# Kernel tuning notes

Hardware: AMD Instinct MI355X
Metric: run time of the kernel (lower is better)

Reference implementation:

```python
import jax, jax.numpy as jnp
import numpy as np

L, D, V = 8, 1024, 32000
DT_MIN, DT_MAX = 0.01, 0.1
EPS = 1e-5


def _layer_norm(x, w, b):
    mu = jnp.mean(x, -1, keepdims=True)
    var = jnp.var(x, -1, keepdims=True)
    return (x - mu) * jax.lax.rsqrt(var + EPS) * w + b


def _encode(ids):
    # deterministic phase encoding of tokens onto the unit phase sphere
    theta = 2.0 * jnp.pi * ids.astype(jnp.float32) / V  # [B,S]
    k = jnp.arange(1, D // 2 + 1, dtype=jnp.float32)
    ang = theta[..., None] * k  # [B,S,D/2]
    return jnp.concatenate([jnp.cos(ang), jnp.sin(ang)], -1) / jnp.sqrt(jnp.float32(D))


def _flux(s, mask):
    # attention-like causal score from state self-interaction
    score = jnp.einsum('bqd,bkd->bqk', s, s) / jnp.sqrt(jnp.float32(D))
    score = jnp.where(mask, score, 0.0)
    return jnp.einsum('bqk,bkd->bqd', score, s), score


def _evolve_with_tunneling(s, dt, mask):
    # Heun-Euler (predictor-corrector) integration step
    k1, score = _flux(s, mask)
    mid = s + dt * k1
    k2, _ = _flux(mid, mask)
    ev = s + 0.5 * dt * (k1 + k2)
    # quantum tunneling: boost low-energy states proportionally to dt/dt_max
    energy = jnp.linalg.norm(ev, axis=-1)  # [B,S]
    thr = jnp.mean(energy, axis=-1, keepdims=True)
    tunnel = energy < thr
    strength = dt / DT_MAX  # [B,1,1]
    ev = jnp.where(tunnel[..., None], ev * (1.0 + strength), ev)
    ratio = jnp.mean(tunnel.astype(jnp.float32))
    return ev, score, ratio


def setup_inputs() -> dict:
    key = jax.random.key(0)
    ks = jax.random.split(key, 4)
    B, S = 2, 2048
    input_ids = jax.random.randint(ks[0], (B, S), 0, V)
    labels = jax.random.randint(ks[1], (B, S), 0, V)
    proj_w = jax.random.normal(ks[2], (L, D, D), jnp.float32) * 0.02
    proj_b = jnp.zeros((L, D), jnp.float32)
    ln_w = jnp.ones((L, D), jnp.float32)
    ln_b = jnp.zeros((L, D), jnp.float32)
    fln_w = jnp.ones((D,), jnp.float32)
    fln_b = jnp.zeros((D,), jnp.float32)
    out_w = jax.random.normal(ks[3], (D, V), jnp.float32) * 0.02
    return dict(input_ids=input_ids, labels=labels, proj_w=proj_w, proj_b=proj_b,
                ln_w=ln_w, ln_b=ln_b, fln_w=fln_w, fln_b=fln_b, out_w=out_w)


def reference(input_ids, labels, proj_w, proj_b, ln_w, ln_b, fln_w, fln_b, out_w):
    B, S = input_ids.shape
    mask = jnp.tril(jnp.ones((S, S), dtype=bool))
    # deterministic timestep (midpoint of [dt_min, dt_max]); dropout in eval mode
    dt = jnp.full((B, 1, 1), 0.5 * (DT_MIN + DT_MAX), jnp.float32)
    states = _encode(input_ids)
    for i in range(L):
        ev, _score, _ratio = _evolve_with_tunneling(states, dt, mask)
        states = _layer_norm(ev @ proj_w[i] + proj_b[i], ln_w[i], ln_b[i])
    states = _layer_norm(states, fln_w, fln_b)
    # normalized quantum projection to vocab
    energy = jnp.linalg.norm(states, axis=-1, keepdims=True)
    logits = (states / (energy + 1e-12)) @ out_w  # [B,S,V]
    # shifted cross-entropy
    sl = logits[:, :-1, :].reshape(-1, V)
    tl = labels[:, 1:].reshape(-1)
    logp = jax.nn.log_softmax(sl, axis=-1)
    loss = -jnp.mean(jnp.take_along_axis(logp, tl[:, None], axis=1))
    return logits, loss
```

## Files before the change

kernel.cpp:

```cpp
#include <hip/hip_runtime.h>

#define LL 8
#define DD 1024
#define VV 32000
#define SS 2048
#define BB 2
#define NROWS 4096
#define DT_STEP 0.055f
#define HALF_DT 0.0275f
#define TUNNEL_SCALE 1.55f

typedef __attribute__((ext_vector_type(8))) short bf16x8;
typedef __attribute__((ext_vector_type(4))) float f32x4;

static __device__ __forceinline__ float bf2f(unsigned short u){
  union { unsigned int i; float f; } v; v.i = ((unsigned int)u) << 16; return v.f;
}
static __device__ __forceinline__ unsigned short f2bf(float f){
  union { float f; unsigned int i; } v; v.f = f;
  unsigned int r = v.i + 0x7fffu + ((v.i >> 16) & 1u);
  return (unsigned short)(r >> 16);
}

static __device__ __forceinline__ void gl16(const unsigned short* g, unsigned short* l){
  __builtin_amdgcn_global_load_lds(
      (const __attribute__((address_space(1))) unsigned int*)g,
      (__attribute__((address_space(3))) unsigned int*)l, 16, 0, 0);
}

__device__ __forceinline__ float block_sum256(float v, volatile float* scratch){
  #pragma unroll
  for (int off = 32; off; off >>= 1) v += __shfl_down(v, off, 64);
  int w = threadIdx.x >> 6, lane = threadIdx.x & 63;
  __syncthreads();
  if (lane == 0) scratch[w] = v;
  __syncthreads();
  return scratch[0] + scratch[1] + scratch[2] + scratch[3];
}

__global__ void encode_kernel(const int* __restrict__ ids, float* __restrict__ s_f32,
                              unsigned short* __restrict__ hi, unsigned short* __restrict__ lo){
  int row = blockIdx.x;
  int t = threadIdx.x;
  float theta = 6.28318530717958647692f * (float)ids[row] / 32000.0f;
  #pragma unroll
  for (int i = 0; i < 2; ++i){
    int kk = t + i * 256;
    float ang = theta * (float)(kk + 1);
    float sv, cv; sincosf(ang, &sv, &cv);
    float c = cv * 0.03125f, s = sv * 0.03125f;
    long b0 = (long)row * DD + kk, b1 = b0 + 512;
    s_f32[b0] = c; s_f32[b1] = s;
    unsigned short ch = f2bf(c); hi[b0] = ch; lo[b0] = f2bf(c - bf2f(ch));
    unsigned short sh = f2bf(s); hi[b1] = sh; lo[b1] = f2bf(s - bf2f(sh));
  }
}

__global__ void transpose_bf16_pair_kernel(const unsigned short* __restrict__ in_hi,
                                           const unsigned short* __restrict__ in_lo,
                                           unsigned short* __restrict__ out_hi,
                                           unsigned short* __restrict__ out_lo,
                                           int R, int C){
  __shared__ __align__(16) unsigned short tile[64][80];
  int zz = blockIdx.z;
  const unsigned short* in = (zz & 1) ? in_lo : in_hi;
  unsigned short* out = (zz & 1) ? out_lo : out_hi;
  long ib = (long)(zz >> 1) * R * C;
  int c0 = blockIdx.x * 64, r0 = blockIdx.y * 64;
  int t = threadIdx.x;
  #pragma unroll
  for (int i = 0; i < 2; ++i){
    int j = t + i * 256; int row = j >> 3, cc = j & 7;
    *(uint4*)&tile[row][cc * 8] = *(const uint4*)(in + ib + (long)(r0 + row) * C + c0 + cc * 8);
  }
  __syncthreads();
  #pragma unroll
  for (int i = 0; i < 2; ++i){
    int j = t + i * 256; int orow = j >> 3, cc = j & 7;
    union { unsigned short u[8]; uint4 v; } tmp;
    #pragma unroll
    for (int e = 0; e < 8; ++e) tmp.u[e] = tile[cc * 8 + e][orow];
    *(uint4*)(out + ib + (long)(c0 + orow) * R + r0 + cc * 8) = tmp.v;
  }
}

template<bool SPLIT>
__global__ void transpose_f32_bf16_kernel(const float* __restrict__ in,
                                          unsigned short* __restrict__ ohi,
                                          unsigned short* __restrict__ olo, int R, int C){
  __shared__ float tile[64][68];
  long ib = (long)blockIdx.z * R * C;
  int c0 = blockIdx.x * 64, r0 = blockIdx.y * 64;
  int t = threadIdx.x;
  #pragma unroll
  for (int i = 0; i < 4; ++i){
    int j = t + i * 256; int row = j >> 4, cc = j & 15;
    *(float4*)&tile[row][cc * 4] = *(const float4*)(in + ib + (long)(r0 + row) * C + c0 + cc * 4);
  }
  __syncthreads();
  #pragma unroll
  for (int i = 0; i < 2; ++i){
    int j = t + i * 256; int orow = j >> 3, cc = j & 7;
    union { unsigned short u[8]; uint4 v; } th, tl;
    #pragma unroll
    for (int e = 0; e < 8; ++e){
      float v = tile[cc * 8 + e][orow];
      unsigned short h = f2bf(v); th.u[e] = h;
      if (SPLIT) tl.u[e] = f2bf(v - bf2f(h));
    }
    long ob = ib + (long)(c0 + orow) * R + r0 + cc * 8;
    *(uint4*)(ohi + ob) = th.v;
    if (SPLIT) *(uint4*)(olo + ob) = tl.v;
  }
}

template<int OUTMODE, int CAUSAL>
__global__ __launch_bounds__(512, 4)
void gemm_nt_kernel(const unsigned short* __restrict__ Ahi, const unsigned short* __restrict__ Alo,
                    const unsigned short* __restrict__ Bhi, const unsigned short* __restrict__ Blo,
                    float* __restrict__ C, unsigned short* __restrict__ Chi,
                    unsigned short* __restrict__ Clo, const float* __restrict__ bias,
                    const float* __restrict__ Sf, const float* __restrict__ K1f,
                    int K, int lda, int ldb, int ldc, int MT, int NT,
                    long batchA, long batchB, long batchC, float alpha)
{
  const int bz = blockIdx.y;
  const int nwg = MT * NT;
  const int q = nwg >> 3, r = nwg & 7;
  const int xcd = blockIdx.x & 7, off = blockIdx.x >> 3;
  const int wg = (xcd < r ? xcd * (q + 1) : r * (q + 1) + (xcd - r) * q) + off;
  const int band = wg / (NT << 3), rem = wg - band * (NT << 3);
  const int mt = (band << 3) + (rem & 7), nt = rem >> 3;
  if (CAUSAL == 1 && nt > mt) return;
  const int m0 = mt << 7, n0 = nt << 7;
  int Keff = K;
  if (CAUSAL == 2){ int kl = (mt + 1) << 7; Keff = kl < K ? kl : K; }

  __shared__ __align__(16) unsigned short sA[2][128][64];
  __shared__ __align__(16) unsigned short sB[2][128][64];

  const int tid = threadIdx.x;
  const int lane = tid & 63;
  const int w = tid >> 6;
  const int wr = w >> 2, wc = w & 3;
  const int fr = lane & 15, fc = lane >> 4;
  const int fr7 = fr & 7;

  f32x4 acc[4][2];
  #pragma unroll
  for (int i = 0; i < 4; ++i)
    #pragma unroll
    for (int j = 0; j < 2; ++j) acc[i][j] = (f32x4){0.f, 0.f, 0.f, 0.f};

  const int srow = tid >> 3, slot = tid & 7;
  const int cont = slot ^ (srow & 7);
  const long aoff = (long)bz * batchA, boff = (long)bz * batchB;
  const int gcol = (cont & 3) << 3;
  const unsigned short* gA = (cont >= 4 ? Alo : Ahi) + aoff + (long)(m0 + srow) * lda + gcol;
  const unsigned short* gB = (cont >= 4 ? Blo : Bhi) + boff + (long)(n0 + srow) * ldb + gcol;
  const long rstepA = 64L * lda, rstepB = 64L * ldb;
  const int wofs = w << 9;

  #define STAGE(buf, kt) do {                                        \
    gl16(gA + (kt),          &sA[buf][0][0] + wofs);                 \
    gl16(gA + (kt) + rstepA, &sA[buf][0][0] + 4096 + wofs);          \
    gl16(gB + (kt),          &sB[buf][0][0] + wofs);                 \
    gl16(gB + (kt) + rstepB, &sB[buf][0][0] + 4096 + wofs);          \
  } while(0)

  const int oh = (fc ^ fr7) << 4;
  const int ol = ((4 + fc) ^ fr7) << 4;

  #define COMPUTE(buf) do {                                                         \
    const char* bA_ = (const char*)&sA[buf][0][0];                                  \
    const char* bB_ = (const char*)&sB[buf][0][0];                                  \
    bf16x8 ah_[4], al_[4];                                                          \
    _Pragma("unroll")                                                               \
    for (int mi = 0; mi < 4; ++mi){                                                 \
      const char* p_ = bA_ + (wr * 64 + mi * 16 + fr) * 128;                        \
      ah_[mi] = *(const bf16x8*)(p_ + oh);                                          \
      al_[mi] = *(const bf16x8*)(p_ + ol);                                          \
    }                                                                               \
    _Pragma("unroll")                                                               \
    for (int ni = 0; ni < 2; ++ni){                                                 \
      const char* pb_ = bB_ + (wc * 32 + ni * 16 + fr) * 128;                       \
      bf16x8 bh_ = *(const bf16x8*)(pb_ + oh);                                      \
      bf16x8 bl_ = *(const bf16x8*)(pb_ + ol);                                      \
      _Pragma("unroll")                                                             \
      for (int mi = 0; mi < 4; ++mi){                                               \
        acc[mi][ni] = __builtin_amdgcn_mfma_f32_16x16x32_bf16(ah_[mi], bh_, acc[mi][ni], 0, 0, 0);\
        acc[mi][ni] = __builtin_amdgcn_mfma_f32_16x16x32_bf16(ah_[mi], bl_, acc[mi][ni], 0, 0, 0);\
        acc[mi][ni] = __builtin_amdgcn_mfma_f32_16x16x32_bf16(al_[mi], bh_, acc[mi][ni], 0, 0, 0);\
      }                                                                             \
    }                                                                               \
  } while(0)

  const int ntiles = Keff >> 5;

  STAGE(0, 0);
  int cur = 0;
  for (int t = 0; t < ntiles - 1; ++t){
    asm volatile("s_barrier" ::: "memory");
    STAGE(cur ^ 1, (t + 1) << 5);
    asm volatile("s_waitcnt vmcnt(4)" ::: "memory");
    asm volatile("s_barrier" ::: "memory");
    COMPUTE(cur);
    cur ^= 1;
  }
  asm volatile("s_waitcnt vmcnt(0)" ::: "memory");
  asm volatile("s_barrier" ::: "memory");
  COMPUTE(cur);

  #undef STAGE
  #undef COMPUTE

  const long coff = (long)bz * batchC;
  const int rb0 = m0 + wr * 64 + fc * 4;
  const int cb0 = n0 + wc * 32 + fr;
  #pragma unroll
  for (int mi = 0; mi < 4; ++mi){
    #pragma unroll
    for (int ni = 0; ni < 2; ++ni){
      #pragma unroll
      for (int rg = 0; rg < 4; ++rg){
        int row = rb0 + mi * 16 + rg;
        int col = cb0 + ni * 16;
        float v = acc[mi][ni][rg] * alpha;
        long idx = coff + (long)row * ldc + col;
        if (OUTMODE == 0){
          if (bias) v += bias[col];
          C[idx] = v;
        } else if (OUTMODE == 2){
          if (CAUSAL == 1 && col > row) v = 0.0f;
          unsigned short h = f2bf(v);
          Chi[idx] = h;
          Clo[idx] = f2bf(v - bf2f(h));
        } else if (OUTMODE == 3){
          C[idx] = v;
          float m = Sf[idx] + DT_STEP * v;
          unsigned short h = f2bf(m);
          Chi[idx] = h;
          Clo[idx] = f2bf(m - bf2f(h));
        } else {
          C[idx] = Sf[idx] + HALF_DT * (K1f[idx] + v);
        }
      }
    }
  }
}

__global__ __launch_bounds__(512, 2)
void gemm256_kernel(const unsigned short* __restrict__ A,
                    const unsigned short* __restrict__ Bt,
                    float* __restrict__ C,
                    float* __restrict__ psum)
{
  const int MT = 16, NT = 125;
  const int nwg = MT * NT;
  const int q = nwg >> 3, r = nwg & 7;
  const int xcd = blockIdx.x & 7, off = blockIdx.x >> 3;
  const int wg = (xcd < r ? xcd * (q + 1) : r * (q + 1) + (xcd - r) * q) + off;
  const int band = wg / (NT << 3), rem = wg - band * (NT << 3);
  const int mt = (band << 3) + (rem & 7), nt = rem >> 3;
  const int m0 = mt << 8, n0 = nt << 8;

  __shared__ __align__(16) unsigned short sA[2][256][64];
  __shared__ __align__(16) unsigned short sB[2][256][64];

  const int tid = threadIdx.x;
  const int lane = tid & 63;
  const int w = tid >> 6;
  const int wr = w >> 2, wc = w & 3;
  const int fr = lane & 15, fc = lane >> 4;
  const int fr7 = fr & 7;

  f32x4 acc[8][4];
  #pragma unroll
  for (int i = 0; i < 8; ++i)
    #pragma unroll
    for (int j = 0; j < 4; ++j) acc[i][j] = (f32x4){0.f, 0.f, 0.f, 0.f};

  const int srow = tid >> 3, slot = tid & 7;
  const int cont = slot ^ (srow & 7);
  const unsigned short* gA = A  + (long)(m0 + srow) * DD + (cont << 3);
  const unsigned short* gB = Bt + (long)(n0 + srow) * DD + (cont << 3);
  const int wofs = w << 9;

  #define SGA(buf, kt, i) gl16(gA + (long)((i) * 64) * DD + (kt), &sA[buf][0][0] + (i) * 4096 + wofs)
  #define SGB(buf, kt, i) gl16(gB + (long)((i) * 64) * DD + (kt), &sB[buf][0][0] + (i) * 4096 + wofs)

  const int oh = (fc ^ fr7) << 4;
  const int ol = ((4 + fc) ^ fr7) << 4;

  #pragma unroll
  for (int i = 0; i < 4; ++i){ SGA(0, 0, i); SGB(0, 0, i); }

  int cur = 0;
  for (int t = 0; t < 16; ++t){
    const int nk = (t + 1) << 6;
    const bool stg = (t < 15);
    const char* bA = (const char*)&sA[cur][0][0];
    const char* bB = (const char*)&sB[cur][0][0];
    bf16x8 aq[4][2], bq[4][2];

    if (stg){ SGA(cur ^ 1, nk, 0); SGA(cur ^ 1, nk, 1);
              asm volatile("s_waitcnt vmcnt(2)" ::: "memory"); }
    else    { asm volatile("s_waitcnt vmcnt(0)" ::: "memory"); }
    asm volatile("s_barrier" ::: "memory");
    #pragma unroll
    for (int mi = 0; mi < 4; ++mi){
      const char* p = bA + (wr * 128 + mi * 16 + fr) * 128;
      aq[mi][0] = *(const bf16x8*)(p + oh);
      aq[mi][1] = *(const bf16x8*)(p + ol);
    }
    #pragma unroll
    for (int ni = 0; ni < 2; ++ni){
      const char* p = bB + (wc * 64 + ni * 16 + fr) * 128;
      bq[ni][0] = *(const bf16x8*)(p + oh);
      bq[ni][1] = *(const bf16x8*)(p + ol);
    }
    __builtin_amdgcn_s_setprio(1);
    #pragma unroll
    for (int ks = 0; ks < 2; ++ks)
      #pragma unroll
      for (int mi = 0; mi < 4; ++mi)
        #pragma unroll
        for (int ni = 0; ni < 2; ++ni)
          acc[mi][ni] = __builtin_amdgcn_mfma_f32_16x16x32_bf16(aq[mi][ks], bq[ni][ks], acc[mi][ni], 0, 0, 0);
    __builtin_amdgcn_s_setprio(0);

    if (stg){ SGA(cur ^ 1, nk, 2); SGA(cur ^ 1, nk, 3); }
    asm volatile("s_barrier" ::: "memory");
    #pragma unroll
    for (int ni = 2; ni < 4; ++ni){
      const char* p = bB + (wc * 64 + ni * 16 + fr) * 128;
      bq[ni][0] = *(const bf16x8*)(p + oh);
      bq[ni][1] = *(const bf16x8*)(p + ol);
    }
    __builtin_amdgcn_s_setprio(1);
    #pragma unroll
    for (int ks = 0; ks < 2; ++ks)
      #pragma unroll
      for (int mi = 0; mi < 4; ++mi)
        #pragma unroll
        for (int ni = 2; ni < 4; ++ni)
          acc[mi][ni] = __builtin_amdgcn_mfma_f32_16x16x32_bf16(aq[mi][ks], bq[ni][ks], acc[mi][ni], 0, 0, 0);
    __builtin_amdgcn_s_setprio(0);

    if (stg){ SGB(cur ^ 1, nk, 0); SGB(cur ^ 1, nk, 1); }
    asm volatile("s_barrier" ::: "memory");
    #pragma unroll
    for (int mi = 0; mi < 4; ++mi){
      const char* p = bA + (wr * 128 + (mi + 4) * 16 + fr) * 128;
      aq[mi][0] = *(const bf16x8*)(p + oh);
      aq[mi][1] = *(const bf16x8*)(p + ol);
    }
    __builtin_amdgcn_s_setprio(1);
    #pragma unroll
    for (int ks = 0; ks < 2; ++ks)
      #pragma unroll
      for (int mi = 0; mi < 4; ++mi)
        #pragma unroll
        for (int ni = 2; ni < 4; ++ni)
          acc[mi + 4][ni] = __builtin_amdgcn_mfma_f32_16x16x32_bf16(aq[mi][ks], bq[ni][ks], acc[mi + 4][ni], 0, 0, 0);
    __builtin_amdgcn_s_setprio(0);

    if (stg){ SGB(cur ^ 1, nk, 2); SGB(cur ^ 1, nk, 3); }
    asm volatile("s_barrier" ::: "memory");
    __builtin_amdgcn_s_setprio(1);
    #pragma unroll
    for (int ks = 0; ks < 2; ++ks)
      #pragma unroll
      for (int mi = 0; mi < 4; ++mi)
        #pragma unroll
        for (int ni = 0; ni < 2; ++ni)
          acc[mi + 4][ni] = __builtin_amdgcn_mfma_f32_16x16x32_bf16(aq[mi][ks], bq[ni][ks], acc[mi + 4][ni], 0, 0, 0);
    __builtin_amdgcn_s_setprio(0);

    cur ^= 1;
  }
  #undef SGA
  #undef SGB

  const int rb0 = m0 + wr * 128 + fc * 4;
  const int cb0 = n0 + wc * 64 + fr;
  #pragma unroll
  for (int mi = 0; mi < 8; ++mi){
    #pragma unroll
    for (int ni = 0; ni < 4; ++ni){
      #pragma unroll
      for (int rg = 0; rg < 4; ++rg){
        C[(long)(rb0 + mi * 16 + rg) * VV + cb0 + ni * 16] = acc[mi][ni][rg];
      }
    }
  }

  #pragma unroll
  for (int mi = 0; mi < 8; ++mi){
    #pragma unroll
    for (int rg = 0; rg < 4; ++rg){
      float s4 = __expf(acc[mi][0][rg]) + __expf(acc[mi][1][rg])
               + __expf(acc[mi][2][rg]) + __expf(acc[mi][3][rg]);
      #pragma unroll
      for (int o = 1; o < 16; o <<= 1) s4 += __shfl_xor(s4, o, 64);
      if (fr == 0){
        long pidx = ((long)(rb0 + mi * 16 + rg) << 9) + nt * 4 + wc;
        psum[pidx] = s4;
      }
    }
  }
}

__global__ void energy_kernel(const float* __restrict__ ev, float* __restrict__ energy){
  int row = blockIdx.x, t = threadIdx.x;
  long base = (long)row * DD + t * 4;
  float4 v = *(const float4*)(ev + base);
  __shared__ float scratch[4];
  float n2 = block_sum256(v.x*v.x + v.y*v.y + v.z*v.z + v.w*v.w, scratch);
  if (t == 0) energy[row] = sqrtf(n2);
}

__global__ void mean_energy_kernel(const float* __restrict__ energy, float* __restrict__ thr){
  int b = blockIdx.x, t = threadIdx.x;
  float s = 0.f;
  for (int j = t; j < SS; j += 256) s += energy[b * SS + j];
  __shared__ float scratch[4];
  float tot = block_sum256(s, scratch);
  if (t == 0) thr[b] = tot * (1.0f / SS);
}

__global__ void tunnel_kernel(const float* __restrict__ ev, const float* __restrict__ energy,
                              const float* __restrict__ thr,
                              unsigned short* __restrict__ hi, unsigned short* __restrict__ lo){
  int row = blockIdx.x, t = threadIdx.x;
  float scale = (energy[row] < thr[row >> 11]) ? TUNNEL_SCALE : 1.0f;
  long base = (long)row * DD + t * 4;
  float4 v = *(const float4*)(ev + base);
  v.x *= scale; v.y *= scale; v.z *= scale; v.w *= scale;
  ushort4 hv, lv;
  hv.x = f2bf(v.x); lv.x = f2bf(v.x - bf2f(hv.x));
  hv.y = f2bf(v.y); lv.y = f2bf(v.y - bf2f(hv.y));
  hv.z = f2bf(v.z); lv.z = f2bf(v.z - bf2f(hv.z));
  hv.w = f2bf(v.w); lv.w = f2bf(v.w - bf2f(hv.w));
  *(ushort4*)(hi + base) = hv; *(ushort4*)(lo + base) = lv;
}

__global__ void ln_kernel(const float* __restrict__ h, const float* __restrict__ w,
                          const float* __restrict__ b, float* __restrict__ s_f32,
                          unsigned short* __restrict__ hi, unsigned short* __restrict__ lo){
  int row = blockIdx.x, t = threadIdx.x;
  long base = (long)row * DD + t * 4;
  float4 xv = *(const float4*)(h + base);
  __shared__ float scratch[4];
  float sum = block_sum256(xv.x + xv.y + xv.z + xv.w, scratch);
  float ssq = block_sum256(xv.x*xv.x + xv.y*xv.y + xv.z*xv.z + xv.w*xv.w, scratch);
  float mu = sum * (1.0f / DD);
  float var = ssq * (1.0f / DD) - mu * mu;
  float rstd = rsqrtf(var + 1e-5f);
  float4 wv = *(const float4*)(w + t * 4), bv = *(const float4*)(b + t * 4);
  float y0 = (xv.x - mu) * rstd * wv.x + bv.x;
  float y1 = (xv.y - mu) * rstd * wv.y + bv.y;
  float y2 = (xv.z - mu) * rstd * wv.z + bv.z;
  float y3 = (xv.w - mu) * rstd * wv.w + bv.w;
  float4 o; o.x = y0; o.y = y1; o.z = y2; o.w = y3;
  *(float4*)(s_f32 + base) = o;
  ushort4 hv, lv;
  hv.x = f2bf(y0); lv.x = f2bf(y0 - bf2f(hv.x));
  hv.y = f2bf(y1); lv.y = f2bf(y1 - bf2f(hv.y));
  hv.z = f2bf(y2); lv.z = f2bf(y2 - bf2f(hv.z));
  hv.w = f2bf(y3); lv.w = f2bf(y3 - bf2f(hv.w));
  *(ushort4*)(hi + base) = hv; *(ushort4*)(lo + base) = lv;
}

__global__ void fln_kernel(const float* __restrict__ s, const float* __restrict__ w,
                           const float* __restrict__ b, unsigned short* __restrict__ uhi){
  int row = blockIdx.x, t = threadIdx.x;
  long base = (long)row * DD + t * 4;
  float4 xv = *(const float4*)(s + base);
  __shared__ float scratch[4];
  float sum = block_sum256(xv.x + xv.y + xv.z + xv.w, scratch);
  float ssq = block_sum256(xv.x*xv.x + xv.y*xv.y + xv.z*xv.z + xv.w*xv.w, scratch);
  float mu = sum * (1.0f / DD);
  float var = ssq * (1.0f / DD) - mu * mu;
  float rstd = rsqrtf(var + 1e-5f);
  float4 wv = *(const float4*)(w + t * 4), bv = *(const float4*)(b + t * 4);
  float y0 = (xv.x - mu) * rstd * wv.x + bv.x;
  float y1 = (xv.y - mu) * rstd * wv.y + bv.y;
  float y2 = (xv.z - mu) * rstd * wv.z + bv.z;
  float y3 = (xv.w - mu) * rstd * wv.w + bv.w;
  float n2 = block_sum256(y0*y0 + y1*y1 + y2*y2 + y3*y3, scratch);
  float inv = 1.0f / (sqrtf(n2) + 1e-12f);
  ushort4 o;
  o.x = f2bf(y0 * inv); o.y = f2bf(y1 * inv);
  o.z = f2bf(y2 * inv); o.w = f2bf(y3 * inv);
  *(ushort4*)(uhi + base) = o;
}

__global__ void lse_reduce_kernel(const float* __restrict__ psum,
                                  const float* __restrict__ logits, const int* __restrict__ labels,
                                  float* __restrict__ lrow){
  int idx = blockIdx.x;
  int b = idx / (SS - 1), qq = idx - b * (SS - 1);
  int row = b * SS + qq;
  int t = threadIdx.x;
  float l = 0.f;
  for (int p = t; p < 500; p += 64) l += psum[((long)row << 9) + p];
  #pragma unroll
  for (int o = 1; o < 64; o <<= 1) l += __shfl_xor(l, o, 64);
  if (t == 0){
    float lse = __logf(l);
    float tl = logits[(long)row * VV + labels[row + 1]];
    lrow[idx] = lse - tl;
  }
}

__global__ void loss_reduce_kernel(const float* __restrict__ lrow, float* __restrict__ dst){
  __shared__ float scratch[4];
  float s = 0.f;
  for (int j = threadIdx.x; j < BB * (SS - 1); j += 256) s += lrow[j];
  float tot = block_sum256(s, scratch);
  if (threadIdx.x == 0) dst[0] = tot / (float)(BB * (SS - 1));
}

extern "C" void kernel_launch(void* const* d_in, const int* in_sizes, int n_in,
                              void* d_out, int out_size, void* d_ws, size_t ws_size,
                              hipStream_t stream) {
  const int*   ids    = (const int*)d_in[0];
  const int*   labels = (const int*)d_in[1];
  const float* proj_w = (const float*)d_in[2];
  const float* proj_b = (const float*)d_in[3];
  const float* ln_w   = (const float*)d_in[4];
  const float* ln_b   = (const float*)d_in[5];
  const float* fln_w  = (const float*)d_in[6];
  const float* fln_b  = (const float*)d_in[7];
  const float* out_w  = (const float*)d_in[8];
  float* out = (float*)d_out;

  char* ws = (char*)d_ws;
  float*          s_f32 = (float*)(ws + 0);
  unsigned short* op_hi = (unsigned short*)(ws + 16777216);
  unsigned short* op_lo = (unsigned short*)(ws + 25165824);
  unsigned short* T_hi  = (unsigned short*)(ws + 33554432);
  unsigned short* T_lo  = (unsigned short*)(ws + 41943040);
  float*          k1    = (float*)(ws + 50331648);
  float*          k2    = (float*)(ws + 67108864);
  unsigned short* sc_hi = (unsigned short*)(ws + 83886080);
  unsigned short* sc_lo = (unsigned short*)(ws + 92274688);
  unsigned short* WhiT  = (unsigned short*)(ws + 100663296);
  unsigned short* WloT  = (unsigned short*)(ws + 117440512);
  float*          energy= (float*)(ws + 134217728);
  float*          thr   = (float*)(ws + 134234112);
  float*          lrow  = (float*)(ws + 134234368);
  unsigned short* owT   = T_hi;
  float*          psum  = (float*)(ws + 0);

  transpose_f32_bf16_kernel<true><<<dim3(16, 16, 8), 256, 0, stream>>>(proj_w, WhiT, WloT, DD, DD);
  encode_kernel<<<NROWS, 256, 0, stream>>>(ids, s_f32, op_hi, op_lo);
  transpose_bf16_pair_kernel<<<dim3(16, 32, 4), 256, 0, stream>>>(op_hi, op_lo, T_hi, T_lo, SS, DD);

  for (int l = 0; l < LL; ++l){
    gemm_nt_kernel<2, 1><<<dim3(256, 2), 512, 0, stream>>>(
        op_hi, op_lo, op_hi, op_lo, nullptr, sc_hi, sc_lo, nullptr, nullptr, nullptr,
        DD, DD, DD, SS, 16, 16, (long)SS * DD, (long)SS * DD, (long)SS * SS, 0.03125f);
    gemm_nt_kernel<3, 2><<<dim3(128, 2), 512, 0, stream>>>(
        sc_hi, sc_lo, T_hi, T_lo, k1, op_hi, op_lo, nullptr, s_f32, nullptr,
        SS, SS, SS, DD, 16, 8, (long)SS * SS, (long)DD * SS, (long)SS * DD, 1.0f);
    transpose_bf16_pair_kernel<<<dim3(16, 32, 4), 256, 0, stream>>>(op_hi, op_lo, T_hi, T_lo, SS, DD);
    gemm_nt_kernel<2, 1><<<dim3(256, 2), 512, 0, stream>>>(
        op_hi, op_lo, op_hi, op_lo, nullptr, sc_hi, sc_lo, nullptr, nullptr, nullptr,
        DD, DD, DD, SS, 16, 16, (long)SS * DD, (long)SS * DD, (long)SS * SS, 0.03125f);
    gemm_nt_kernel<4, 2><<<dim3(128, 2), 512, 0, stream>>>(
        sc_hi, sc_lo, T_hi, T_lo, k2, nullptr, nullptr, nullptr, s_f32, k1,
        SS, SS, SS, DD, 16, 8, (long)SS * SS, (long)DD * SS, (long)SS * DD, 1.0f);
    energy_kernel<<<NROWS, 256, 0, stream>>>(k2, energy);
    mean_energy_kernel<<<BB, 256, 0, stream>>>(energy, thr);
    tunnel_kernel<<<NROWS, 256, 0, stream>>>(k2, energy, thr, op_hi, op_lo);
    gemm_nt_kernel<0, 0><<<dim3(256, 1), 512, 0, stream>>>(
        op_hi, op_lo, WhiT + (long)l * DD * DD, WloT + (long)l * DD * DD,
        k1, nullptr, nullptr, proj_b + l * DD, nullptr, nullptr,
        DD, DD, DD, DD, 32, 8, 0, 0, 0, 1.0f);
    ln_kernel<<<NROWS, 256, 0, stream>>>(k1, ln_w + l * DD, ln_b + l * DD, s_f32, op_hi, op_lo);
    if (l < LL - 1){
      transpose_bf16_pair_kernel<<<dim3(16, 32, 4), 256, 0, stream>>>(op_hi, op_lo, T_hi, T_lo, SS, DD);
    }
  }

  transpose_f32_bf16_kernel<false><<<dim3(500, 16, 1), 256, 0, stream>>>(out_w, owT, nullptr, DD, VV);
  fln_kernel<<<NROWS, 256, 0, stream>>>(s_f32, fln_w, fln_b, op_hi);
  gemm256_kernel<<<2000, 512, 0, stream>>>(op_hi, owT, out, psum);
  lse_reduce_kernel<<<BB * (SS - 1), 64, 0, stream>>>(psum, out, labels, lrow);
  loss_reduce_kernel<<<1, 256, 0, stream>>>(lrow, out + (long)NROWS * VV);
}
```

Measured before the change: 2.939 ms.

## Split GEMM k-loop into two half-phases interleaving loads, barriers and MFMA

The software-pipelined bf16x3 GEMM main loop is restructured so each k-tile is processed in two halves. The next tile's A loads are issued before the first barrier and its B loads between the two halves, which spreads global-to-LDS traffic across the MFMA work and removes the separate epilogue iteration. MFMA blocks are wrapped in s_setprio raises to favor the compute wave. In exchange the loop now has a conditional staging branch, and correctness depends on careful vmcnt/barrier ordering for the double buffers.

```diff
diff --git a/kernel.cpp b/kernel.cpp
--- a/kernel.cpp
+++ b/kernel.cpp
@@ -161,58 +161,72 @@
   const long rstepA = 64L * lda, rstepB = 64L * ldb;
   const int wofs = w << 9;
 
-  #define STAGE(buf, kt) do {                                        \
-    gl16(gA + (kt),          &sA[buf][0][0] + wofs);                 \
-    gl16(gA + (kt) + rstepA, &sA[buf][0][0] + 4096 + wofs);          \
-    gl16(gB + (kt),          &sB[buf][0][0] + wofs);                 \
-    gl16(gB + (kt) + rstepB, &sB[buf][0][0] + 4096 + wofs);          \
-  } while(0)
-
   const int oh = (fc ^ fr7) << 4;
   const int ol = ((4 + fc) ^ fr7) << 4;
 
-  #define COMPUTE(buf) do {                                                         \
-    const char* bA_ = (const char*)&sA[buf][0][0];                                  \
-    const char* bB_ = (const char*)&sB[buf][0][0];                                  \
-    bf16x8 ah_[4], al_[4];                                                          \
-    _Pragma("unroll")                                                               \
-    for (int mi = 0; mi < 4; ++mi){                                                 \
-      const char* p_ = bA_ + (wr * 64 + mi * 16 + fr) * 128;                        \
-      ah_[mi] = *(const bf16x8*)(p_ + oh);                                          \
-      al_[mi] = *(const bf16x8*)(p_ + ol);                                          \
-    }                                                                               \
-    _Pragma("unroll")                                                               \
-    for (int ni = 0; ni < 2; ++ni){                                                 \
-      const char* pb_ = bB_ + (wc * 32 + ni * 16 + fr) * 128;                       \
-      bf16x8 bh_ = *(const bf16x8*)(pb_ + oh);                                      \
-      bf16x8 bl_ = *(const bf16x8*)(pb_ + ol);                                      \
-      _Pragma("unroll")                                                             \
-      for (int mi = 0; mi < 4; ++mi){                                               \
-        acc[mi][ni] = __builtin_amdgcn_mfma_f32_16x16x32_bf16(ah_[mi], bh_, acc[mi][ni], 0, 0, 0);\
-        acc[mi][ni] = __builtin_amdgcn_mfma_f32_16x16x32_bf16(ah_[mi], bl_, acc[mi][ni], 0, 0, 0);\
-        acc[mi][ni] = __builtin_amdgcn_mfma_f32_16x16x32_bf16(al_[mi], bh_, acc[mi][ni], 0, 0, 0);\
-      }                                                                             \
-    }                                                                               \
-  } while(0)
-
   const int ntiles = Keff >> 5;
 
-  STAGE(0, 0);
+  gl16(gA,          &sA[0][0][0] + wofs);
+  gl16(gA + rstepA, &sA[0][0][0] + 4096 + wofs);
+  gl16(gB,          &sB[0][0][0] + wofs);
+  gl16(gB + rstepB, &sB[0][0][0] + 4096 + wofs);
+
   int cur = 0;
-  for (int t = 0; t < ntiles - 1; ++t){
+  for (int t = 0; t < ntiles; ++t){
+    const bool stg = (t < ntiles - 1);
+    const long nk = (long)(t + 1) << 5;
+    const char* bA_ = (const char*)&sA[cur][0][0];
+    const char* bB_ = (const char*)&sB[cur][0][0];
+    bf16x8 ah_[4], al_[4];
+
+    if (stg){
+      gl16(gA + nk,          &sA[cur ^ 1][0][0] + wofs);
+      gl16(gA + nk + rstepA, &sA[cur ^ 1][0][0] + 4096 + wofs);
+      asm volatile("s_waitcnt vmcnt(2)" ::: "memory");
+    } else {
+      asm volatile("s_waitcnt vmcnt(0)" ::: "memory");
+    }
     asm volatile("s_barrier" ::: "memory");
-    STAGE(cur ^ 1, (t + 1) << 5);
-    asm volatile("s_waitcnt vmcnt(4)" ::: "memory");
+    #pragma unroll
+    for (int mi = 0; mi < 4; ++mi){
+      const char* p_ = bA_ + (wr * 64 + mi * 16 + fr) * 128;
+      ah_[mi] = *(const bf16x8*)(p_ + oh);
+      al_[mi] = *(const bf16x8*)(p_ + ol);
+    }
+    {
+      const char* pb_ = bB_ + (wc * 32 + fr) * 128;
+      bf16x8 bh_ = *(const bf16x8*)(pb_ + oh);
+      bf16x8 bl_ = *(const bf16x8*)(pb_ + ol);
+      __builtin_amdgcn_s_setprio(1);
+      #pragma unroll
+      for (int mi = 0; mi < 4; ++mi){
+        acc[mi][0] = __builtin_amdgcn_mfma_f32_16x16x32_bf16(ah_[mi], bh_, acc[mi][0], 0, 0, 0);
+        acc[mi][0] = __builtin_amdgcn_mfma_f32_16x16x32_bf16(ah_[mi], bl_, acc[mi][0], 0, 0, 0);
+        acc[mi][0] = __builtin_amdgcn_mfma_f32_16x16x32_bf16(al_[mi], bh_, acc[mi][0], 0, 0, 0);
+      }
+      __builtin_amdgcn_s_setprio(0);
+    }
+
+    if (stg){
+      gl16(gB + nk,          &sB[cur ^ 1][0][0] + wofs);
+      gl16(gB + nk + rstepB, &sB[cur ^ 1][0][0] + 4096 + wofs);
+    }
     asm volatile("s_barrier" ::: "memory");
-    COMPUTE(cur);
+    {
+      const char* pb_ = bB_ + (wc * 32 + 16 + fr) * 128;
+      bf16x8 bh_ = *(const bf16x8*)(pb_ + oh);
+      bf16x8 bl_ = *(const bf16x8*)(pb_ + ol);
+      __builtin_amdgcn_s_setprio(1);
+      #pragma unroll
+      for (int mi = 0; mi < 4; ++mi){
+        acc[mi][1] = __builtin_amdgcn_mfma_f32_16x16x32_bf16(ah_[mi], bh_, acc[mi][1], 0, 0, 0);
+        acc[mi][1] = __builtin_amdgcn_mfma_f32_16x16x32_bf16(ah_[mi], bl_, acc[mi][1], 0, 0, 0);
+        acc[mi][1] = __builtin_amdgcn_mfma_f32_16x16x32_bf16(al_[mi], bh_, acc[mi][1], 0, 0, 0);
+      }
+      __builtin_amdgcn_s_setprio(0);
+    }
     cur ^= 1;
   }
-  asm volatile("s_waitcnt vmcnt(0)" ::: "memory");
-  asm volatile("s_barrier" ::: "memory");
-  COMPUTE(cur);
-
-  #undef STAGE
-  #undef COMPUTE
 
   const long coff = (long)bz * batchC;
   const int rb0 = m0 + wr * 64 + fc * 4;
```

New measurement: 2.826 ms. 1.04x faster.
